# Performance work log

Hardware: AMD Instinct MI355X
Metric: run time of the kernel (lower is better)

Reference implementation:

```python
import jax, jax.numpy as jnp
import numpy as np

ALPHA = 0.5      # sklearn Lasso(alpha=0.5)
N_ITERS = 50     # fixed FISTA iterations
N_POWER = 10     # power iterations for Lipschitz estimate


def _soft(x, thr):
    return jnp.sign(x) * jnp.maximum(jnp.abs(x) - thr, 0.0)


def setup_inputs() -> dict:
    key = jax.random.key(0)
    k1, k2 = jax.random.split(key)
    B, n_rx, n_tx, n_carrier = 8, 4, 32, 256
    M = 256
    D = n_rx * n_tx * n_carrier * 2  # 65536
    x = jax.random.normal(k1, (B, n_rx, n_tx, n_carrier, 2), jnp.float32)
    coding_mat = jax.random.normal(k2, (B, M, D), jnp.float32)
    return {"x": x, "coding_mat": coding_mat}


def _lasso_fista(x, coding_mat):
    B = x.shape[0]
    M = coding_mat.shape[1]
    D = coding_mat.shape[2]
    shape = x.shape
    w_true = x.reshape(B, D)                       # (nrx ntx channel complex) flatten
    y = jnp.einsum('bmd,bd->bm', coding_mat, w_true)  # compressed measurements

    # Lipschitz constant of grad of (1/(2M))||y - Aw||^2 via power iteration on A^T A / M
    def power_step(_, v):
        Av = jnp.einsum('bmd,bd->bm', coding_mat, v)
        v = jnp.einsum('bmd,bm->bd', coding_mat, Av)
        return v / (jnp.linalg.norm(v, axis=-1, keepdims=True) + 1e-12)

    v = jnp.full((B, D), 1.0 / np.sqrt(D), dtype=x.dtype)
    v = jax.lax.fori_loop(0, N_POWER, power_step, v)
    Av = jnp.einsum('bmd,bd->bm', coding_mat, v)
    L = jnp.einsum('bm,bm->b', Av, Av) / M        # rayleigh quotient, v unit norm
    L = jax.lax.stop_gradient(L)[:, None]          # [B,1] step-size constant

    w0 = jnp.zeros((B, D), x.dtype)

    def fista_step(carry, _):
        w, z, t = carry
        r = jnp.einsum('bmd,bd->bm', coding_mat, z) - y
        grad = jnp.einsum('bmd,bm->bd', coding_mat, r) / M
        w_new = _soft(z - grad / L, ALPHA / L)
        t_new = 0.5 * (1.0 + jnp.sqrt(1.0 + 4.0 * t * t))
        z_new = w_new + ((t - 1.0) / t_new) * (w_new - w)
        return (w_new, z_new, t_new), None

    (w, _, _), _ = jax.lax.scan(fista_step, (w0, w0, jnp.float32(1.0)), None, length=N_ITERS)
    return w.reshape(shape)


def reference(x, coding_mat):
    return _lasso_fista(x, coding_mat)
```

## Files before the change

### kernel.cpp

```cpp
#include <hip/hip_runtime.h>
#include <hip/hip_fp16.h>
#include <math.h>

#define B 8
#define M 256
#define D 65536
#define NCH 512

static constexpr float ALPHA = 0.5f;
static constexpr int N_ITERS = 50;
static constexpr int N_POWER = 10;

typedef _Float16 f16x8 __attribute__((ext_vector_type(8)));
typedef float f32x4 __attribute__((ext_vector_type(4)));


__global__ __launch_bounds__(256) void k_conv(const float* __restrict__ A,
                                              __half* __restrict__ Aht) {
    const size_t n8 = (size_t)B * M * D / 8;
    size_t stride = (size_t)gridDim.x * 256;
    for (size_t i = (size_t)blockIdx.x * 256 + threadIdx.x; i < n8; i += stride) {
        float4 f0 = ((const float4*)A)[2 * i];
        float4 f1 = ((const float4*)A)[2 * i + 1];
        union { uint4 u; __half2 h[4]; } o;
        o.h[0] = __floats2half2_rn(f0.x, f0.y);
        o.h[1] = __floats2half2_rn(f0.z, f0.w);
        o.h[2] = __floats2half2_rn(f1.x, f1.y);
        o.h[3] = __floats2half2_rn(f1.z, f1.w);
        size_t d8 = i & (D / 8 - 1);
        size_t m  = (i >> 13) & (M - 1);
        size_t b  = i >> 21;
        size_t ch = d8 >> 4;
        size_t dlo8 = d8 & 15;
        ((uint4*)Aht)[(((b * NCH + ch) * M + m) << 4) + dlo8] = o.u;
    }
}

__global__ __launch_bounds__(256) void k_ypart(const __half* __restrict__ Aht,
                                               const float* __restrict__ x,
                                               float* __restrict__ ypart,
                                               float* __restrict__ upart) {
    int cid = blockIdx.x;
    int b = cid >> 9;
    int ch = cid & (NCH - 1);
    int t = threadIdx.x;
    int dj = t & 15;
    int mi = t >> 4;

    __shared__ float xs[128];
    __shared__ float sredY[M];
    __shared__ float sredU[M];
    if (t < 32)
        ((float4*)xs)[t] = ((const float4*)(x + (size_t)b * D + ch * 128))[t];
    __syncthreads();

    float zr[8];
    {
        float4 z0 = *(const float4*)&xs[dj * 8];
        float4 z1 = *(const float4*)&xs[dj * 8 + 4];
        zr[0] = z0.x; zr[1] = z0.y; zr[2] = z0.z; zr[3] = z0.w;
        zr[4] = z1.x; zr[5] = z1.y; zr[6] = z1.z; zr[7] = z1.w;
    }

    const __half* Ap = Aht + (((size_t)b * NCH + ch) * M + mi) * 128 + dj * 8;
#pragma unroll
    for (int s = 0; s < 16; ++s) {
        uint4 a = *(const uint4*)(Ap + (size_t)(s * 16) * 128);
        const __half2* hp = (const __half2*)&a;
        float2 f0 = __half22float2(hp[0]);
        float2 f1 = __half22float2(hp[1]);
        float2 f2 = __half22float2(hp[2]);
        float2 f3 = __half22float2(hp[3]);
        float p = f0.x * zr[0] + f0.y * zr[1] + f1.x * zr[2] + f1.y * zr[3] +
                  f2.x * zr[4] + f2.y * zr[5] + f3.x * zr[6] + f3.y * zr[7];
        float q = f0.x + f0.y + f1.x + f1.y + f2.x + f2.y + f3.x + f3.y;
        p += __shfl_xor(p, 1, 64); q += __shfl_xor(q, 1, 64);
        p += __shfl_xor(p, 2, 64); q += __shfl_xor(q, 2, 64);
        p += __shfl_xor(p, 4, 64); q += __shfl_xor(q, 4, 64);
        p += __shfl_xor(p, 8, 64); q += __shfl_xor(q, 8, 64);
        if (dj == 0) { sredY[s * 16 + mi] = p; sredU[s * 16 + mi] = q; }
    }
    __syncthreads();
    ypart[((size_t)b * NCH + ch) * M + t] = sredY[t];
    upart[((size_t)b * NCH + ch) * M + t] = sredU[t];
}

__global__ __launch_bounds__(256) void k_yred(const float* __restrict__ ypart,
                                              const float* __restrict__ upart,
                                              float* __restrict__ y,
                                              float* __restrict__ u) {
    int blk = blockIdx.x;
    int b = blk >> 3;
    int mg = blk & 7;
    int t = threadIdx.x;
    int tm = t & 31;
    int cg = t >> 5;
    int m = mg * 32 + tm;
    const float* yp = ypart + (size_t)b * NCH * M + m;
    const float* up = upart + (size_t)b * NCH * M + m;
    float sy = 0.f, su = 0.f;
#pragma unroll 8
    for (int ch = cg; ch < NCH; ch += 8) {
        sy += yp[(size_t)ch * M];
        su += up[(size_t)ch * M];
    }
    __shared__ float redY[8][32], redU[8][32];
    redY[cg][tm] = sy; redU[cg][tm] = su;
    __syncthreads();
    if (t < 32) {
        float vy = 0.f, vu = 0.f;
#pragma unroll
        for (int g = 0; g < 8; ++g) { vy += redY[g][t]; vu += redU[g][t]; }
        int bm = b * M + mg * 32 + t;
        y[bm] = vy;
        u[bm] = vu * 0.00390625f;
    }
}

__global__ __launch_bounds__(256) void k_gram_mfma(const __half* __restrict__ Aht,
                                                   float* __restrict__ G) {
    int bx = blockIdx.x;
    int ch2 = bx & 31;
    int p  = (bx >> 5) % 3;
    int b  = bx / 96;
    const int PI[3] = {0, 0, 128};
    const int PJ[3] = {0, 128, 128};
    int ti = PI[p], tj = PJ[p];
    int k0 = ch2 * 2048;

    __shared__ __half As[128 * 32];
    __shared__ __half Bs[128 * 32];

    int t = threadIdx.x;
    int w = t >> 6, lane = t & 63;
    int wr = w >> 1, wc = w & 1;

    int srow = w * 32 + (lane >> 2);
    int scol = (lane & 3) * 8;

    f32x4 acc[4][4];
#pragma unroll
    for (int i = 0; i < 4; ++i)
#pragma unroll
        for (int j = 0; j < 4; ++j)
            acc[i][j] = (f32x4){0.f, 0.f, 0.f, 0.f};

    int frow = lane & 15;
    int koff = (lane >> 4) * 8;

    const size_t bbase = (size_t)b * NCH;
    for (int ks = 0; ks < 2048; ks += 32) {
        int d = k0 + ks;
        size_t chb = bbase + (d >> 7);
        int dlo = d & 127;
        __syncthreads();
        {
            const __half* ga0 = Aht + (chb * M + (ti + srow)) * 128 + dlo + scol;
            const __half* ga1 = ga0 + 16 * 128;
            const __half* gb0 = Aht + (chb * M + (tj + srow)) * 128 + dlo + scol;
            const __half* gb1 = gb0 + 16 * 128;
            __builtin_amdgcn_global_load_lds(
                (const __attribute__((address_space(1))) void*)ga0,
                (__attribute__((address_space(3))) void*)&As[(w * 32) * 32], 16, 0, 0);
            __builtin_amdgcn_global_load_lds(
                (const __attribute__((address_space(1))) void*)ga1,
                (__attribute__((address_space(3))) void*)&As[(w * 32 + 16) * 32], 16, 0, 0);
            __builtin_amdgcn_global_load_lds(
                (const __attribute__((address_space(1))) void*)gb0,
                (__attribute__((address_space(3))) void*)&Bs[(w * 32) * 32], 16, 0, 0);
            __builtin_amdgcn_global_load_lds(
                (const __attribute__((address_space(1))) void*)gb1,
                (__attribute__((address_space(3))) void*)&Bs[(w * 32 + 16) * 32], 16, 0, 0);
        }
        __syncthreads();

        f16x8 aF[4], bF[4];
#pragma unroll
        for (int i = 0; i < 4; ++i)
            aF[i] = *(const f16x8*)&As[(wr * 64 + i * 16 + frow) * 32 + koff];
#pragma unroll
        for (int j = 0; j < 4; ++j)
            bF[j] = *(const f16x8*)&Bs[(wc * 64 + j * 16 + frow) * 32 + koff];
#pragma unroll
        for (int i = 0; i < 4; ++i)
#pragma unroll
            for (int j = 0; j < 4; ++j)
                acc[i][j] = __builtin_amdgcn_mfma_f32_16x16x32_f16(
                    aF[i], bF[j], acc[i][j], 0, 0, 0);
    }

    float* Gb = G + (size_t)b * M * M;
    bool offd = (ti != tj);
    int r0 = (lane >> 4) * 4;
    int c0 = lane & 15;
#pragma unroll
    for (int i = 0; i < 4; ++i)
#pragma unroll
        for (int j = 0; j < 4; ++j)
#pragma unroll
            for (int r = 0; r < 4; ++r) {
                int gi = ti + wr * 64 + i * 16 + r0 + r;
                int gj = tj + wc * 64 + j * 16 + c0;
                float v = acc[i][j][r];
                atomicAdd(&Gb[(size_t)gi * M + gj], v);
                if (offd) atomicAdd(&Gb[(size_t)gj * M + gi], v);
            }
}

__global__ __launch_bounds__(256) void k_power(const float* __restrict__ G,
                                               const float* __restrict__ u0,
                                               float* __restrict__ Lp) {
    int b = blockIdx.x;
    int m = threadIdx.x;
    __shared__ float su[M];
    __shared__ float red[4];
    su[m] = u0[b * M + m];
    __syncthreads();
    const float* Gb = G + (size_t)b * M * M;
    for (int it = 0; it < N_POWER; ++it) {
        float gm = 0.f;
        const float4* grow = (const float4*)(Gb + (size_t)m * M);
#pragma unroll 8
        for (int k = 0; k < M / 4; ++k) {
            float4 g = grow[k];
            gm += g.x * su[4 * k] + g.y * su[4 * k + 1] + g.z * su[4 * k + 2] +
                  g.w * su[4 * k + 3];
        }
        float part = su[m] * gm;
        for (int off = 32; off > 0; off >>= 1) part += __shfl_down(part, off, 64);
        if ((m & 63) == 0) red[m >> 6] = part;
        __syncthreads();
        float n = sqrtf(red[0] + red[1] + red[2] + red[3]);
        float inv = 1.f / (n + 1e-12f);
        su[m] = gm * inv;
        __syncthreads();
    }
    float part = su[m] * su[m];
    for (int off = 32; off > 0; off >>= 1) part += __shfl_down(part, off, 64);
    if ((m & 63) == 0) red[m >> 6] = part;
    __syncthreads();
    if (m == 0) {
        float L = (red[0] + red[1] + red[2] + red[3]) * (1.0f / 256.0f);
        Lp[b * 4 + 0] = L;
        Lp[b * 4 + 1] = 1.0f / (256.0f * L);
        Lp[b * 4 + 2] = ALPHA / L;
    }
}

__global__ __launch_bounds__(256) void k_cstep(const float* __restrict__ spart,
                                               const float* __restrict__ y,
                                               const float* __restrict__ Lp,
                                               float* __restrict__ c) {
    int blk = blockIdx.x;
    int b = blk >> 3;
    int mg = blk & 7;
    int t = threadIdx.x;
    int tm = t & 31;
    int cg = t >> 5;
    int m = mg * 32 + tm;
    const float* sp = spart + (size_t)b * NCH * M + m;
    float s = 0.f;
#pragma unroll 8
    for (int ch = cg; ch < NCH; ch += 8)
        s += sp[(size_t)ch * M];
    __shared__ float red[8][32];
    red[cg][tm] = s;
    __syncthreads();
    if (t < 32) {
        float sv = red[0][t] + red[1][t] + red[2][t] + red[3][t] +
                   red[4][t] + red[5][t] + red[6][t] + red[7][t];
        int bm = b * M + mg * 32 + t;
        c[bm] = (sv - y[bm]) * Lp[b * 4 + 1];
    }
}

__global__ __launch_bounds__(256) void k_fista(const __half* __restrict__ Aht,
                                               const float* __restrict__ cc,
                                               const float* __restrict__ Lp,
                                               float* __restrict__ z,
                                               float* __restrict__ w,
                                               float* __restrict__ spart,
                                               float beta) {
    int cid = blockIdx.x;
    int b = cid >> 9;
    int chunk = cid & (NCH - 1);
    int d0 = chunk << 7;
    int t = threadIdx.x;
    int dj = t & 15;
    int mi = t >> 4;

    __shared__ float sc[M];
    __shared__ float gws[4][16][8];
    __shared__ float znS[128];
    __shared__ float sred[M];

    sc[t] = cc[b * M + t];
    __syncthreads();

    const __half* Ap = Aht + (((size_t)b * NCH + chunk) * M + mi) * 128 + dj * 8;
    uint4 areg[16];
    float g[8] = {};
#pragma unroll
    for (int s = 0; s < 16; ++s) {
        areg[s] = *(const uint4*)(Ap + (size_t)(s * 16) * 128);
        float cm = sc[s * 16 + mi];
        const __half2* hp = (const __half2*)&areg[s];
        float2 f0 = __half22float2(hp[0]);
        float2 f1 = __half22float2(hp[1]);
        float2 f2 = __half22float2(hp[2]);
        float2 f3 = __half22float2(hp[3]);
        g[0] = fmaf(f0.x, cm, g[0]); g[1] = fmaf(f0.y, cm, g[1]);
        g[2] = fmaf(f1.x, cm, g[2]); g[3] = fmaf(f1.y, cm, g[3]);
        g[4] = fmaf(f2.x, cm, g[4]); g[5] = fmaf(f2.y, cm, g[5]);
        g[6] = fmaf(f3.x, cm, g[6]); g[7] = fmaf(f3.y, cm, g[7]);
    }
#pragma unroll
    for (int j = 0; j < 8; ++j) {
        g[j] += __shfl_xor(g[j], 16, 64);
        g[j] += __shfl_xor(g[j], 32, 64);
    }
    int wv = t >> 6;
    if ((t & 63) < 16) {
#pragma unroll
        for (int j = 0; j < 8; ++j) gws[wv][dj][j] = g[j];
    }
    __syncthreads();

    if (t < 128) {
        int ldj = t >> 3, lj = t & 7;
        float gs = gws[0][ldj][lj] + gws[1][ldj][lj] +
                   gws[2][ldj][lj] + gws[3][ldj][lj];
        size_t zi = (size_t)b * D + d0 + t;
        float thr = Lp[b * 4 + 2];
        float zv = z[zi], wold = w[zi];
        float cand = zv - gs;
        float a1 = fabsf(cand) - thr;
        float wn = a1 > 0.f ? copysignf(a1, cand) : 0.f;
        float znv = wn + beta * (wn - wold);
        w[zi] = wn;
        z[zi] = znv;
        znS[t] = znv;
    }
    __syncthreads();

    float zr[8];
    {
        float4 z0 = *(const float4*)&znS[dj * 8];
        float4 z1 = *(const float4*)&znS[dj * 8 + 4];
        zr[0] = z0.x; zr[1] = z0.y; zr[2] = z0.z; zr[3] = z0.w;
        zr[4] = z1.x; zr[5] = z1.y; zr[6] = z1.z; zr[7] = z1.w;
    }
#pragma unroll
    for (int s = 0; s < 16; ++s) {
        const __half2* hp = (const __half2*)&areg[s];
        float2 f0 = __half22float2(hp[0]);
        float2 f1 = __half22float2(hp[1]);
        float2 f2 = __half22float2(hp[2]);
        float2 f3 = __half22float2(hp[3]);
        float p = f0.x * zr[0] + f0.y * zr[1] + f1.x * zr[2] + f1.y * zr[3] +
                  f2.x * zr[4] + f2.y * zr[5] + f3.x * zr[6] + f3.y * zr[7];
        p += __shfl_xor(p, 1, 64);
        p += __shfl_xor(p, 2, 64);
        p += __shfl_xor(p, 4, 64);
        p += __shfl_xor(p, 8, 64);
        if (dj == 0) sred[s * 16 + mi] = p;
    }
    __syncthreads();
    spart[((size_t)b * NCH + chunk) * M + t] = sred[t];
}

extern "C" void kernel_launch(void* const* d_in, const int* in_sizes, int n_in,
                              void* d_out, int out_size, void* d_ws, size_t ws_size,
                              hipStream_t stream) {
    (void)in_sizes; (void)n_in; (void)out_size; (void)ws_size;
    const float* x = (const float*)d_in[0];
    const float* A = (const float*)d_in[1];
    float* w = (float*)d_out;

    __half* Aht = (__half*)d_ws;
    float* ws = (float*)((char*)d_ws + (size_t)B * M * D * sizeof(__half));
    float* y  = ws;
    float* u  = ws + 2048;
    float* Lp = ws + 4096;
    float* c  = ws + 4128;
    float* z  = ws + 8192;
    float* G  = ws + 8192 + 524288;
    float* spart = G;
    float* ypart = spart + (size_t)B * NCH * M;
    float* upart = ypart + (size_t)B * NCH * M;

    hipMemsetAsync(G, 0, (size_t)B * M * M * sizeof(float), stream);
    hipMemsetAsync(z, 0, (size_t)B * D * sizeof(float), stream);
    hipMemsetAsync(w, 0, (size_t)B * D * sizeof(float), stream);

    k_conv<<<16384, 256, 0, stream>>>(A, Aht);
    k_ypart<<<B * NCH, 256, 0, stream>>>(Aht, x, ypart, upart);
    k_yred<<<64, 256, 0, stream>>>(ypart, upart, y, u);
    k_gram_mfma<<<8 * 3 * 32, 256, 0, stream>>>(Aht, G);
    k_power<<<B, 256, 0, stream>>>(G, u, Lp);

    hipMemsetAsync(spart, 0, (size_t)B * NCH * M * sizeof(float), stream);

    double t = 1.0;
    for (int k = 0; k < N_ITERS; ++k) {
        double tn = 0.5 * (1.0 + sqrt(1.0 + 4.0 * t * t));
        float beta = (float)((t - 1.0) / tn);
        k_cstep<<<64, 256, 0, stream>>>(spart, y, Lp, c);
        k_fista<<<B * NCH, 256, 0, stream>>>(Aht, c, Lp, z, w, spart, beta);
        t = tn;
    }
}
```

Baseline: 3.707 ms.

## Fuse fp16 conversion with y partial sums; process two chunks per FISTA block

The fp32-to-fp16 conversion kernel now iterates in output order, reading A strided and writing Aht contiguously, and computes the y and u partial dot products from the freshly converted values. This removes the separate k_ypart pass that reread Aht. The FISTA kernel now launches half as many blocks, and each block loops over two chunks. That amortises the c load and threshold fetch but halves the parallelism of the per-iteration kernel.

```diff
diff --git a/kernel.cpp b/kernel.cpp
--- a/kernel.cpp
+++ b/kernel.cpp
@@ -15,74 +15,47 @@
 typedef float f32x4 __attribute__((ext_vector_type(4)));
 
 
-__global__ __launch_bounds__(256) void k_conv(const float* __restrict__ A,
-                                              __half* __restrict__ Aht) {
+__global__ __launch_bounds__(256) void k_conv_y(const float* __restrict__ A,
+                                                const float* __restrict__ x,
+                                                __half* __restrict__ Aht,
+                                                float* __restrict__ ypart,
+                                                float* __restrict__ upart) {
     const size_t n8 = (size_t)B * M * D / 8;
     size_t stride = (size_t)gridDim.x * 256;
     for (size_t i = (size_t)blockIdx.x * 256 + threadIdx.x; i < n8; i += stride) {
-        float4 f0 = ((const float4*)A)[2 * i];
-        float4 f1 = ((const float4*)A)[2 * i + 1];
+        size_t dlo8 = i & 15;
+        size_t m  = (i >> 4) & (M - 1);
+        size_t ch = (i >> 12) & (NCH - 1);
+        size_t b  = i >> 21;
+        size_t in8 = (b << 21) | (m << 13) | (ch << 4) | dlo8;
+        float4 f0 = ((const float4*)A)[2 * in8];
+        float4 f1 = ((const float4*)A)[2 * in8 + 1];
         union { uint4 u; __half2 h[4]; } o;
         o.h[0] = __floats2half2_rn(f0.x, f0.y);
         o.h[1] = __floats2half2_rn(f0.z, f0.w);
         o.h[2] = __floats2half2_rn(f1.x, f1.y);
         o.h[3] = __floats2half2_rn(f1.z, f1.w);
-        size_t d8 = i & (D / 8 - 1);
-        size_t m  = (i >> 13) & (M - 1);
-        size_t b  = i >> 21;
-        size_t ch = d8 >> 4;
-        size_t dlo8 = d8 & 15;
-        ((uint4*)Aht)[(((b * NCH + ch) * M + m) << 4) + dlo8] = o.u;
-    }
-}
-
-__global__ __launch_bounds__(256) void k_ypart(const __half* __restrict__ Aht,
-                                               const float* __restrict__ x,
-                                               float* __restrict__ ypart,
-                                               float* __restrict__ upart) {
-    int cid = blockIdx.x;
-    int b = cid >> 9;
-    int ch = cid & (NCH - 1);
-    int t = threadIdx.x;
-    int dj = t & 15;
-    int mi = t >> 4;
-
-    __shared__ float xs[128];
-    __shared__ float sredY[M];
-    __shared__ float sredU[M];
-    if (t < 32)
-        ((float4*)xs)[t] = ((const float4*)(x + (size_t)b * D + ch * 128))[t];
-    __syncthreads();
-
-    float zr[8];
-    {
-        float4 z0 = *(const float4*)&xs[dj * 8];
-        float4 z1 = *(const float4*)&xs[dj * 8 + 4];
-        zr[0] = z0.x; zr[1] = z0.y; zr[2] = z0.z; zr[3] = z0.w;
-        zr[4] = z1.x; zr[5] = z1.y; zr[6] = z1.z; zr[7] = z1.w;
-    }
-
-    const __half* Ap = Aht + (((size_t)b * NCH + ch) * M + mi) * 128 + dj * 8;
-#pragma unroll
-    for (int s = 0; s < 16; ++s) {
-        uint4 a = *(const uint4*)(Ap + (size_t)(s * 16) * 128);
-        const __half2* hp = (const __half2*)&a;
-        float2 f0 = __half22float2(hp[0]);
-        float2 f1 = __half22float2(hp[1]);
-        float2 f2 = __half22float2(hp[2]);
-        float2 f3 = __half22float2(hp[3]);
-        float p = f0.x * zr[0] + f0.y * zr[1] + f1.x * zr[2] + f1.y * zr[3] +
-                  f2.x * zr[4] + f2.y * zr[5] + f3.x * zr[6] + f3.y * zr[7];
-        float q = f0.x + f0.y + f1.x + f1.y + f2.x + f2.y + f3.x + f3.y;
+        ((uint4*)Aht)[i] = o.u;
+
+        const float4* xp =
+            (const float4*)(x + ((b << 16) | (ch << 7) | (dlo8 << 3)));
+        float4 x0 = xp[0], x1 = xp[1];
+        float2 g0 = __half22float2(o.h[0]);
+        float2 g1 = __half22float2(o.h[1]);
+        float2 g2 = __half22float2(o.h[2]);
+        float2 g3 = __half22float2(o.h[3]);
+        float p = g0.x * x0.x + g0.y * x0.y + g1.x * x0.z + g1.y * x0.w +
+                  g2.x * x1.x + g2.y * x1.y + g3.x * x1.z + g3.y * x1.w;
+        float q = g0.x + g0.y + g1.x + g1.y + g2.x + g2.y + g3.x + g3.y;
         p += __shfl_xor(p, 1, 64); q += __shfl_xor(q, 1, 64);
         p += __shfl_xor(p, 2, 64); q += __shfl_xor(q, 2, 64);
         p += __shfl_xor(p, 4, 64); q += __shfl_xor(q, 4, 64);
         p += __shfl_xor(p, 8, 64); q += __shfl_xor(q, 8, 64);
-        if (dj == 0) { sredY[s * 16 + mi] = p; sredU[s * 16 + mi] = q; }
-    }
-    __syncthreads();
-    ypart[((size_t)b * NCH + ch) * M + t] = sredY[t];
-    upart[((size_t)b * NCH + ch) * M + t] = sredU[t];
+        if (dlo8 == 0) {
+            ypart[i >> 4] = p;
+            upart[i >> 4] = q;
+        }
+    }
 }
 
 __global__ __launch_bounds__(256) void k_yred(const float* __restrict__ ypart,
@@ -282,9 +255,8 @@
                                                float* __restrict__ spart,
                                                float beta) {
     int cid = blockIdx.x;
-    int b = cid >> 9;
-    int chunk = cid & (NCH - 1);
-    int d0 = chunk << 7;
+    int b = cid >> 8;
+    int pair = cid & 255;
     int t = threadIdx.x;
     int dj = t & 15;
     int mi = t >> 4;
@@ -296,77 +268,84 @@
 
     sc[t] = cc[b * M + t];
     __syncthreads();
-
-    const __half* Ap = Aht + (((size_t)b * NCH + chunk) * M + mi) * 128 + dj * 8;
-    uint4 areg[16];
-    float g[8] = {};
-#pragma unroll
-    for (int s = 0; s < 16; ++s) {
-        areg[s] = *(const uint4*)(Ap + (size_t)(s * 16) * 128);
-        float cm = sc[s * 16 + mi];
-        const __half2* hp = (const __half2*)&areg[s];
-        float2 f0 = __half22float2(hp[0]);
-        float2 f1 = __half22float2(hp[1]);
-        float2 f2 = __half22float2(hp[2]);
-        float2 f3 = __half22float2(hp[3]);
-        g[0] = fmaf(f0.x, cm, g[0]); g[1] = fmaf(f0.y, cm, g[1]);
-        g[2] = fmaf(f1.x, cm, g[2]); g[3] = fmaf(f1.y, cm, g[3]);
-        g[4] = fmaf(f2.x, cm, g[4]); g[5] = fmaf(f2.y, cm, g[5]);
-        g[6] = fmaf(f3.x, cm, g[6]); g[7] = fmaf(f3.y, cm, g[7]);
-    }
-#pragma unroll
-    for (int j = 0; j < 8; ++j) {
-        g[j] += __shfl_xor(g[j], 16, 64);
-        g[j] += __shfl_xor(g[j], 32, 64);
-    }
-    int wv = t >> 6;
-    if ((t & 63) < 16) {
-#pragma unroll
-        for (int j = 0; j < 8; ++j) gws[wv][dj][j] = g[j];
-    }
-    __syncthreads();
-
-    if (t < 128) {
-        int ldj = t >> 3, lj = t & 7;
-        float gs = gws[0][ldj][lj] + gws[1][ldj][lj] +
-                   gws[2][ldj][lj] + gws[3][ldj][lj];
-        size_t zi = (size_t)b * D + d0 + t;
-        float thr = Lp[b * 4 + 2];
-        float zv = z[zi], wold = w[zi];
-        float cand = zv - gs;
-        float a1 = fabsf(cand) - thr;
-        float wn = a1 > 0.f ? copysignf(a1, cand) : 0.f;
-        float znv = wn + beta * (wn - wold);
-        w[zi] = wn;
-        z[zi] = znv;
-        znS[t] = znv;
-    }
-    __syncthreads();
-
-    float zr[8];
-    {
-        float4 z0 = *(const float4*)&znS[dj * 8];
-        float4 z1 = *(const float4*)&znS[dj * 8 + 4];
-        zr[0] = z0.x; zr[1] = z0.y; zr[2] = z0.z; zr[3] = z0.w;
-        zr[4] = z1.x; zr[5] = z1.y; zr[6] = z1.z; zr[7] = z1.w;
-    }
-#pragma unroll
-    for (int s = 0; s < 16; ++s) {
-        const __half2* hp = (const __half2*)&areg[s];
-        float2 f0 = __half22float2(hp[0]);
-        float2 f1 = __half22float2(hp[1]);
-        float2 f2 = __half22float2(hp[2]);
-        float2 f3 = __half22float2(hp[3]);
-        float p = f0.x * zr[0] + f0.y * zr[1] + f1.x * zr[2] + f1.y * zr[3] +
-                  f2.x * zr[4] + f2.y * zr[5] + f3.x * zr[6] + f3.y * zr[7];
-        p += __shfl_xor(p, 1, 64);
-        p += __shfl_xor(p, 2, 64);
-        p += __shfl_xor(p, 4, 64);
-        p += __shfl_xor(p, 8, 64);
-        if (dj == 0) sred[s * 16 + mi] = p;
-    }
-    __syncthreads();
-    spart[((size_t)b * NCH + chunk) * M + t] = sred[t];
+    float thr = Lp[b * 4 + 2];
+
+    for (int half = 0; half < 2; ++half) {
+        int chunk = pair * 2 + half;
+        int d0 = chunk << 7;
+
+        const __half* Ap =
+            Aht + (((size_t)b * NCH + chunk) * M + mi) * 128 + dj * 8;
+        uint4 areg[16];
+        float g[8] = {};
+#pragma unroll
+        for (int s = 0; s < 16; ++s) {
+            areg[s] = *(const uint4*)(Ap + (size_t)(s * 16) * 128);
+            float cm = sc[s * 16 + mi];
+            const __half2* hp = (const __half2*)&areg[s];
+            float2 f0 = __half22float2(hp[0]);
+            float2 f1 = __half22float2(hp[1]);
+            float2 f2 = __half22float2(hp[2]);
+            float2 f3 = __half22float2(hp[3]);
+            g[0] = fmaf(f0.x, cm, g[0]); g[1] = fmaf(f0.y, cm, g[1]);
+            g[2] = fmaf(f1.x, cm, g[2]); g[3] = fmaf(f1.y, cm, g[3]);
+            g[4] = fmaf(f2.x, cm, g[4]); g[5] = fmaf(f2.y, cm, g[5]);
+            g[6] = fmaf(f3.x, cm, g[6]); g[7] = fmaf(f3.y, cm, g[7]);
+        }
+#pragma unroll
+        for (int j = 0; j < 8; ++j) {
+            g[j] += __shfl_xor(g[j], 16, 64);
+            g[j] += __shfl_xor(g[j], 32, 64);
+        }
+        int wv = t >> 6;
+        if ((t & 63) < 16) {
+#pragma unroll
+            for (int j = 0; j < 8; ++j) gws[wv][dj][j] = g[j];
+        }
+        __syncthreads();
+
+        if (t < 128) {
+            int ldj = t >> 3, lj = t & 7;
+            float gs = gws[0][ldj][lj] + gws[1][ldj][lj] +
+                       gws[2][ldj][lj] + gws[3][ldj][lj];
+            size_t zi = (size_t)b * D + d0 + t;
+            float zv = z[zi], wold = w[zi];
+            float cand = zv - gs;
+            float a1 = fabsf(cand) - thr;
+            float wn = a1 > 0.f ? copysignf(a1, cand) : 0.f;
+            float znv = wn + beta * (wn - wold);
+            w[zi] = wn;
+            z[zi] = znv;
+            znS[t] = znv;
+        }
+        __syncthreads();
+
+        float zr[8];
+        {
+            float4 z0 = *(const float4*)&znS[dj * 8];
+            float4 z1 = *(const float4*)&znS[dj * 8 + 4];
+            zr[0] = z0.x; zr[1] = z0.y; zr[2] = z0.z; zr[3] = z0.w;
+            zr[4] = z1.x; zr[5] = z1.y; zr[6] = z1.z; zr[7] = z1.w;
+        }
+#pragma unroll
+        for (int s = 0; s < 16; ++s) {
+            const __half2* hp = (const __half2*)&areg[s];
+            float2 f0 = __half22float2(hp[0]);
+            float2 f1 = __half22float2(hp[1]);
+            float2 f2 = __half22float2(hp[2]);
+            float2 f3 = __half22float2(hp[3]);
+            float p = f0.x * zr[0] + f0.y * zr[1] + f1.x * zr[2] +
+                      f1.y * zr[3] + f2.x * zr[4] + f2.y * zr[5] +
+                      f3.x * zr[6] + f3.y * zr[7];
+            p += __shfl_xor(p, 1, 64);
+            p += __shfl_xor(p, 2, 64);
+            p += __shfl_xor(p, 4, 64);
+            p += __shfl_xor(p, 8, 64);
+            if (dj == 0) sred[s * 16 + mi] = p;
+        }
+        __syncthreads();
+        spart[((size_t)b * NCH + chunk) * M + t] = sred[t];
+    }
 }
 
 extern "C" void kernel_launch(void* const* d_in, const int* in_sizes, int n_in,
@@ -393,8 +372,7 @@
     hipMemsetAsync(z, 0, (size_t)B * D * sizeof(float), stream);
     hipMemsetAsync(w, 0, (size_t)B * D * sizeof(float), stream);
 
-    k_conv<<<16384, 256, 0, stream>>>(A, Aht);
-    k_ypart<<<B * NCH, 256, 0, stream>>>(Aht, x, ypart, upart);
+    k_conv_y<<<16384, 256, 0, stream>>>(A, x, Aht, ypart, upart);
     k_yred<<<64, 256, 0, stream>>>(ypart, upart, y, u);
     k_gram_mfma<<<8 * 3 * 32, 256, 0, stream>>>(Aht, G);
     k_power<<<B, 256, 0, stream>>>(G, u, Lp);
@@ -406,7 +384,7 @@
         double tn = 0.5 * (1.0 + sqrt(1.0 + 4.0 * t * t));
         float beta = (float)((t - 1.0) / tn);
         k_cstep<<<64, 256, 0, stream>>>(spart, y, Lp, c);
-        k_fista<<<B * NCH, 256, 0, stream>>>(Aht, c, Lp, z, w, spart, beta);
+        k_fista<<<2048, 256, 0, stream>>>(Aht, c, Lp, z, w, spart, beta);
         t = tn;
     }
 }
```

After: 3.965 ms. 7.0% more time.
